# Kernel optimization log

Hardware: AMD Instinct MI355X
Metric: run time of the kernel (lower is better)

The kernel has to match this reference:

```python
import jax, jax.numpy as jnp
import numpy as np

T = 0.1        # temperature
MARGIN = 0.0   # margin m
NEG_IOU = 0.5  # negative iou threshold
K = 2          # pos_topk
WEIGHT = 1.0


def _l2norm(x, eps=1e-12):
    n = jnp.sqrt(jnp.sum(x * x, axis=-1, keepdims=True))
    return x / jnp.maximum(n, eps)


def setup_inputs() -> dict:
    key = jax.random.key(0)
    k0, k1, k2, k3 = jax.random.split(key, 4)
    B, C, N = 8, 256, 128
    s_per, m_per = 4, 2          # sentences per video, targets per sentence
    S, M = B * s_per, B * s_per * m_per
    video_feats = jax.random.normal(k0, (B, C, N, N), dtype=jnp.float32)
    sents_feats = jax.random.normal(k1, (S, C), dtype=jnp.float32)
    num_sentences = jnp.full((B,), s_per, dtype=jnp.int32)
    num_targets = jnp.full((S,), m_per, dtype=jnp.int32)
    iou2d = jax.random.uniform(k2, (S, N, N), dtype=jnp.float32)
    iou2ds = jax.random.uniform(k3, (M, N, N), dtype=jnp.float32)
    mask2d = jnp.asarray(np.triu(np.ones((N, N), dtype=bool)))
    return {"video_feats": video_feats, "sents_feats": sents_feats,
            "num_sentences": num_sentences, "num_targets": num_targets,
            "iou2d": iou2d, "iou2ds": iou2ds, "mask2d": mask2d}


def reference(video_feats, sents_feats, num_sentences, num_targets, iou2d, iou2ds, mask2d):
    B, C, N, _ = video_feats.shape
    S = iou2d.shape[0]
    M = iou2ds.shape[0]
    P = N * (N + 1) // 2  # number of valid proposals in upper-triangular mask2d
    flat_idx = jnp.nonzero(mask2d.reshape(-1), size=P)[0]

    # masked_select -> (B, P, C) proposal features, l2-normalized over C
    vf = video_feats.reshape(B, C, N * N)[:, :, flat_idx].transpose(0, 2, 1)
    vf = _l2norm(vf)
    sf = _l2norm(sents_feats)  # normalized as in original (unused downstream)
    iou2d_p = iou2d.reshape(S, -1)[:, flat_idx]    # (S, P)
    iou2ds_p = iou2ds.reshape(M, -1)[:, flat_idx]  # (M, P)

    s_per = S // B  # uniform sentences per video (static)
    m_per = M // S  # uniform targets per sentence (static)
    scatter_s2v = jnp.repeat(jnp.arange(B), s_per)    # (S,)
    scatter_m2s = jnp.repeat(jnp.arange(S), m_per)    # (M,)
    scatter_m2v = scatter_s2v[scatter_m2s]            # (M,)

    # top-K proposals per target moment by iou2ds
    topk_idx = jax.lax.top_k(iou2ds_p, K)[1]  # (M, K)
    topk_feats = jnp.take_along_axis(vf[scatter_m2v], topk_idx[:, :, None], axis=1)  # (M,K,C)
    pos_feats = topk_feats.reshape(M * K, C)

    # all (ref, pos) pairs within each sentence's m_per*K selected proposals
    mK = m_per * K
    a = jnp.arange(mK)
    shifts = jnp.arange(S) * mK
    ref_idx = (shifts[:, None] + jnp.repeat(a, mK)[None, :]).reshape(-1)  # (E,)
    pos_idx = (shifts[:, None] + jnp.tile(a, mK)[None, :]).reshape(-1)    # (E,)
    scatter_e2s = jnp.repeat(jnp.arange(S), mK * mK)                      # (E,)

    intra_pos = jnp.sum(pos_feats[ref_idx] * pos_feats[pos_idx], axis=-1)  # (E,)
    intra_all = pos_feats @ vf.reshape(-1, C).T                            # (M*K, B*P)

    # neg mask: within own video, exclude proposals with iou > NEG_IOU; other videos all negative
    own = scatter_s2v[:, None] == jnp.arange(B)[None, :]                   # (S, B)
    pos_mask = (own[:, :, None] & (iou2d_p > NEG_IOU)[:, None, :]).reshape(S, B * P)
    neg_mask = ~pos_mask

    ps = intra_pos
    all_s = intra_all[ref_idx]           # (E, B*P)
    nm = neg_mask[scatter_e2s]           # (E, B*P)
    pos_exp = jnp.exp((ps - MARGIN) / T)
    neg_sum = jnp.sum(jnp.exp(all_s / T) * nm, axis=-1)
    loss = jnp.mean(-((ps - MARGIN) / T - jnp.log(pos_exp + neg_sum)))
    return loss * WEIGHT
```

## Files before the change

kernel.cpp:

```cpp
#include <hip/hip_runtime.h>
#include <math.h>

#define NN    128
#define NN2   16384
#define CDIM  256
#define BV    8
#define MM    64
#define RR    128
#define PP    8256
#define NBLK  1032
#define BPB   129
#define TEMP  0.1f
#define NEGIOU 0.5f

typedef __attribute__((ext_vector_type(8))) short bf16x8;
typedef __attribute__((ext_vector_type(4))) float f32x4;

static __device__ __forceinline__ unsigned short f2bf(float x) {
    union { float f; unsigned u; } c; c.f = x;
    unsigned r = c.u + 0x7FFFu + ((c.u >> 16) & 1u);
    return (unsigned short)(r >> 16);
}

__global__ __launch_bounds__(256) void topk_part_kernel(const float* __restrict__ iou2ds,
                                                        float* __restrict__ pv,
                                                        int* __restrict__ pk) {
    int m = blockIdx.x, q = blockIdx.y, tid = threadIdx.x;
    const float* src = iou2ds + (size_t)m * NN2;
    float v1 = -1e30f, v2 = -1e30f;
    int k1 = 0x7fffffff, k2 = 0x7fffffff;
    int base = q * 4096;
#pragma unroll
    for (int i = 0; i < 16; ++i) {
        int k = base + tid + 256 * i;
        int r = k >> 7, c = k & 127;
        if (c < r) continue;
        float v = src[k];
        if (v > v1 || (v == v1 && k < k1)) { v2 = v1; k2 = k1; v1 = v; k1 = k; }
        else if (v > v2 || (v == v2 && k < k2)) { v2 = v; k2 = k; }
    }
    __shared__ float sv[512];  __shared__ int sk[512];
    __shared__ float sv2[128]; __shared__ int sk2[128];
    sv[tid * 2] = v1; sv[tid * 2 + 1] = v2;
    sk[tid * 2] = k1; sk[tid * 2 + 1] = k2;
    __syncthreads();
    if (tid < 64) {
        float b1 = -1e30f, b2 = -1e30f; int c1 = 0x7fffffff, c2 = 0x7fffffff;
        for (int t = tid * 8; t < tid * 8 + 8; ++t) {
            float v = sv[t]; int k = sk[t];
            if (v > b1 || (v == b1 && k < c1)) { b2 = b1; c2 = c1; b1 = v; c1 = k; }
            else if (v > b2 || (v == b2 && k < c2)) { b2 = v; c2 = k; }
        }
        sv2[tid * 2] = b1; sv2[tid * 2 + 1] = b2;
        sk2[tid * 2] = c1; sk2[tid * 2 + 1] = c2;
    }
    __syncthreads();
    if (tid == 0) {
        float b1 = -1e30f, b2 = -1e30f; int c1 = 0x7fffffff, c2 = 0x7fffffff;
        for (int t = 0; t < 128; ++t) {
            float v = sv2[t]; int k = sk2[t];
            if (v > b1 || (v == b1 && k < c1)) { b2 = b1; c2 = c1; b1 = v; c1 = k; }
            else if (v > b2 || (v == b2 && k < c2)) { b2 = v; c2 = k; }
        }
        pv[(m * 4 + q) * 2] = b1; pv[(m * 4 + q) * 2 + 1] = b2;
        pk[(m * 4 + q) * 2] = c1; pk[(m * 4 + q) * 2 + 1] = c2;
    }
}

__global__ __launch_bounds__(64) void posfeat_kernel(const float* __restrict__ vfeat,
                                                     const float* __restrict__ pv,
                                                     const int* __restrict__ pk,
                                                     float* __restrict__ pos,
                                                     unsigned short* __restrict__ posFrag) {
    int r = blockIdx.x, lane = threadIdx.x;
    int m = r >> 1, b = m >> 3, kk = r & 1;
    float b1 = -1e30f, b2 = -1e30f; int c1 = 0x7fffffff, c2 = 0x7fffffff;
    for (int t = 0; t < 8; ++t) {
        float v = pv[m * 8 + t]; int k = pk[m * 8 + t];
        if (v > b1 || (v == b1 && k < c1)) { b2 = b1; c2 = c1; b1 = v; c1 = k; }
        else if (v > b2 || (v == b2 && k < c2)) { b2 = v; c2 = k; }
    }
    int ij = kk ? c2 : c1;
    const float* base = vfeat + (size_t)b * CDIM * NN2 + ij;
    float v[4];
    float ss = 0.0f;
#pragma unroll
    for (int q = 0; q < 4; ++q) {
        int c = lane + 64 * q;
        v[q] = base[(size_t)c * NN2];
        ss += v[q] * v[q];
    }
#pragma unroll
    for (int o = 32; o > 0; o >>= 1) ss += __shfl_xor(ss, o, 64);
    float inv = 1.0f / fmaxf(sqrtf(ss), 1e-12f);
#pragma unroll
    for (int q = 0; q < 4; ++q) {
        int c = lane + 64 * q;
        float val = v[q] * inv;
        pos[r * CDIM + c] = val;
        int idx = (((c >> 5) * 8 + (r >> 4)) * 64 + ((r & 15) | (((c >> 3) & 3) << 4))) * 8 + (c & 7);
        posFrag[idx] = f2bf(val);
    }
}

__global__ __launch_bounds__(512, 4) void neg_kernel(const float* __restrict__ vfeat,
                                                     const float* __restrict__ iou2d,
                                                     const unsigned short* __restrict__ posFrag,
                                                     float* __restrict__ part) {
    __shared__ unsigned short sB[2][2][4][64][8];
    __shared__ int   sIJ[64];
    __shared__ int   sMask[64];
    __shared__ float sNP[8][64];
    __shared__ float sInv[64];
    __shared__ float sNeg[RR];

    int tid = threadIdx.x;
    int bid = blockIdx.x;
    int b   = bid / BPB;
    int p0  = (bid - b * BPB) * 64;

    if (tid < RR) sNeg[tid] = 0.0f;
    if (tid < 64) {
        int p = p0 + tid;
        int i = (int)((257.0f - sqrtf(66049.0f - 8.0f * (float)p)) * 0.5f);
        if (i < 0) i = 0;
        while ((i + 1) * (257 - (i + 1)) / 2 <= p) ++i;
        while (i * (257 - i) / 2 > p) --i;
        int j = p - i * (257 - i) / 2 + i;
        int ij = i * NN + j;
        sIJ[tid] = ij;
        int mask = 0;
#pragma unroll
        for (int t = 0; t < 4; ++t) {
            float iv = iou2d[((size_t)(4 * b + t)) * NN2 + ij];
            mask |= (iv > NEGIOU) ? (1 << t) : 0;
        }
        sMask[tid] = mask;
    }

    int lane = tid & 63;
    int col  = tid & 63;
    int wv   = tid >> 6;
    int rowgroup = wv >> 1;
    int colgroup = wv & 1;

    bf16x8 afrag[2][8];
    const bf16x8* pf = (const bf16x8*)posFrag;
#pragma unroll
    for (int mt = 0; mt < 2; ++mt)
#pragma unroll
        for (int s = 0; s < 8; ++s)
            afrag[mt][s] = pf[(s * 8 + rowgroup * 2 + mt) * 64 + lane];

    __syncthreads();

    const float* vcol = vfeat + (size_t)b * CDIM * NN2 + sIJ[col];

    f32x4 acc[2][2];
#pragma unroll
    for (int mt = 0; mt < 2; ++mt)
#pragma unroll
        for (int nt = 0; nt < 2; ++nt)
#pragma unroll
            for (int e = 0; e < 4; ++e) acc[mt][nt][e] = 0.0f;

    float nrm = 0.0f;
    float r[8];
#pragma unroll
    for (int j = 0; j < 8; ++j) r[j] = vcol[(size_t)(wv * 8 + j) * NN2];

    int s_loc = wv >> 2;
    int slot  = (col & 15) | ((wv & 3) << 4);
    int nt_w  = col >> 4;

    for (int ph = 0; ph < 4; ++ph) {
        union { bf16x8 v; unsigned u[4]; } pkd;
#pragma unroll
        for (int j = 0; j < 4; ++j)
            pkd.u[j] = (unsigned)f2bf(r[2 * j]) | ((unsigned)f2bf(r[2 * j + 1]) << 16);
#pragma unroll
        for (int j = 0; j < 8; ++j) nrm = fmaf(r[j], r[j], nrm);
        *(bf16x8*)&sB[ph & 1][s_loc][nt_w][slot][0] = pkd.v;
        __syncthreads();
        if (ph < 3) {
#pragma unroll
            for (int j = 0; j < 8; ++j)
                r[j] = vcol[(size_t)((ph + 1) * 64 + wv * 8 + j) * NN2];
        }
#pragma unroll
        for (int s = 0; s < 2; ++s)
#pragma unroll
            for (int ntl = 0; ntl < 2; ++ntl) {
                bf16x8 bfrag = *(const bf16x8*)&sB[ph & 1][s][colgroup * 2 + ntl][lane][0];
#pragma unroll
                for (int mt = 0; mt < 2; ++mt)
                    acc[mt][ntl] = __builtin_amdgcn_mfma_f32_16x16x32_bf16(
                        afrag[mt][ph * 2 + s], bfrag, acc[mt][ntl], 0, 0, 0);
            }
    }

    sNP[wv][col] = nrm;
    __syncthreads();
    if (tid < 64) {
        float s = 0.0f;
        for (int t = 0; t < 8; ++t) s += sNP[t][tid];
        sInv[tid] = 10.0f / fmaxf(sqrtf(s), 1e-12f);
    }
    __syncthreads();

#pragma unroll
    for (int mt = 0; mt < 2; ++mt)
#pragma unroll
        for (int ntl = 0; ntl < 2; ++ntl)
#pragma unroll
            for (int reg = 0; reg < 4; ++reg) {
                int row = rowgroup * 32 + mt * 16 + ((lane >> 4) << 2) + reg;
                int cl  = colgroup * 32 + ntl * 16 + (lane & 15);
                float e = __expf(acc[mt][ntl][reg] * sInv[cl]);
                int excl = ((row >> 4) == b) & ((sMask[cl] >> ((row >> 2) & 3)) & 1);
                e = excl ? 0.0f : e;
#pragma unroll
                for (int off = 1; off < 16; off <<= 1) e += __shfl_xor(e, off, 64);
                if ((lane & 15) == 0) atomicAdd(&sNeg[row], e);
            }
    __syncthreads();
    if (tid < RR) part[(size_t)tid * NBLK + bid] = sNeg[tid];
}

__global__ __launch_bounds__(256) void reduce_kernel(const float* __restrict__ part,
                                                     float* __restrict__ neg) {
    int r = blockIdx.x, tid = threadIdx.x;
    const float* row = part + (size_t)r * NBLK;
    float s = 0.0f;
    for (int t = tid; t < NBLK; t += 256) s += row[t];
#pragma unroll
    for (int o = 32; o > 0; o >>= 1) s += __shfl_xor(s, o, 64);
    __shared__ float sw[4];
    if ((tid & 63) == 0) sw[tid >> 6] = s;
    __syncthreads();
    if (tid == 0) neg[r] = sw[0] + sw[1] + sw[2] + sw[3];
}

__global__ __launch_bounds__(256) void loss_kernel(const float* __restrict__ pos,
                                                   const float* __restrict__ neg,
                                                   float* __restrict__ out) {
    int tid = threadIdx.x;
    float local = 0.0f;
    for (int e = tid; e < 512; e += 256) {
        int s  = e >> 4;
        int aa = (e >> 2) & 3;
        int bb = e & 3;
        int rr = s * 4 + aa;
        int pp = s * 4 + bb;
        const float4* pr = (const float4*)(pos + rr * CDIM);
        const float4* pq = (const float4*)(pos + pp * CDIM);
        float dot = 0.0f;
        for (int c = 0; c < CDIM / 4; ++c) {
            float4 a = pr[c], bv = pq[c];
            dot += a.x * bv.x + a.y * bv.y + a.z * bv.z + a.w * bv.w;
        }
        float x = dot / TEMP;
        local += logf(__expf(x) + neg[rr]) - x;
    }
#pragma unroll
    for (int o = 32; o > 0; o >>= 1) local += __shfl_xor(local, o, 64);
    __shared__ float sred[4];
    if ((tid & 63) == 0) sred[tid >> 6] = local;
    __syncthreads();
    if (tid == 0) out[0] = (sred[0] + sred[1] + sred[2] + sred[3]) / 512.0f;
}

extern "C" void kernel_launch(void* const* d_in, const int* in_sizes, int n_in,
                              void* d_out, int out_size, void* d_ws, size_t ws_size,
                              hipStream_t stream) {
    (void)in_sizes; (void)n_in; (void)out_size; (void)ws_size;
    const float* vfeat  = (const float*)d_in[0];
    const float* iou2d  = (const float*)d_in[4];
    const float* iou2ds = (const float*)d_in[5];

    float* ws = (float*)d_ws;
    float*          pos     = ws;
    unsigned short* posFrag = (unsigned short*)(ws + 32768);
    float*          pv      = ws + 32768 + 16384;
    int*            pk      = (int*)(pv + 512);
    float*          part    = pv + 1024;
    float*          neg     = part + RR * NBLK;

    topk_part_kernel<<<dim3(MM, 4), 256, 0, stream>>>(iou2ds, pv, pk);
    posfeat_kernel  <<<RR, 64, 0, stream>>>(vfeat, pv, pk, pos, posFrag);
    neg_kernel      <<<NBLK, 512, 0, stream>>>(vfeat, iou2d, posFrag, part);
    reduce_kernel   <<<RR, 256, 0, stream>>>(part, neg);
    loss_kernel     <<<1, 256, 0, stream>>>(pos, neg, (float*)d_out);
}
```

Baseline: 257.0 us.

## Fuse topk with posfeat and reduce with loss via last-block atomic counter

```diff
diff --git a/kernel.cpp b/kernel.cpp
--- a/kernel.cpp
+++ b/kernel.cpp
@@ -22,25 +22,27 @@
     return (unsigned short)(r >> 16);
 }
 
-__global__ __launch_bounds__(256) void topk_part_kernel(const float* __restrict__ iou2ds,
-                                                        float* __restrict__ pv,
-                                                        int* __restrict__ pk) {
-    int m = blockIdx.x, q = blockIdx.y, tid = threadIdx.x;
+__global__ __launch_bounds__(256) void prep_kernel(const float* __restrict__ vfeat,
+                                                   const float* __restrict__ iou2ds,
+                                                   float* __restrict__ pos,
+                                                   unsigned short* __restrict__ posFrag,
+                                                   int* __restrict__ done) {
+    int m = blockIdx.x, tid = threadIdx.x;
+    if (m == 0 && tid == 0) *done = 0;
+
     const float* src = iou2ds + (size_t)m * NN2;
     float v1 = -1e30f, v2 = -1e30f;
     int k1 = 0x7fffffff, k2 = 0x7fffffff;
-    int base = q * 4096;
-#pragma unroll
-    for (int i = 0; i < 16; ++i) {
-        int k = base + tid + 256 * i;
-        int r = k >> 7, c = k & 127;
-        if (c < r) continue;
+    for (int k = tid; k < NN2; k += 256) {
+        int i = k >> 7, j = k & 127;
+        if (j < i) continue;
         float v = src[k];
         if (v > v1 || (v == v1 && k < k1)) { v2 = v1; k2 = k1; v1 = v; k1 = k; }
         else if (v > v2 || (v == v2 && k < k2)) { v2 = v; k2 = k; }
     }
     __shared__ float sv[512];  __shared__ int sk[512];
     __shared__ float sv2[128]; __shared__ int sk2[128];
+    __shared__ int sTop[2];
     sv[tid * 2] = v1; sv[tid * 2 + 1] = v2;
     sk[tid * 2] = k1; sk[tid * 2 + 1] = k2;
     __syncthreads();
@@ -62,45 +64,33 @@
             if (v > b1 || (v == b1 && k < c1)) { b2 = b1; c2 = c1; b1 = v; c1 = k; }
             else if (v > b2 || (v == b2 && k < c2)) { b2 = v; c2 = k; }
         }
-        pv[(m * 4 + q) * 2] = b1; pv[(m * 4 + q) * 2 + 1] = b2;
-        pk[(m * 4 + q) * 2] = c1; pk[(m * 4 + q) * 2 + 1] = c2;
-    }
-}
-
-__global__ __launch_bounds__(64) void posfeat_kernel(const float* __restrict__ vfeat,
-                                                     const float* __restrict__ pv,
-                                                     const int* __restrict__ pk,
-                                                     float* __restrict__ pos,
-                                                     unsigned short* __restrict__ posFrag) {
-    int r = blockIdx.x, lane = threadIdx.x;
-    int m = r >> 1, b = m >> 3, kk = r & 1;
-    float b1 = -1e30f, b2 = -1e30f; int c1 = 0x7fffffff, c2 = 0x7fffffff;
-    for (int t = 0; t < 8; ++t) {
-        float v = pv[m * 8 + t]; int k = pk[m * 8 + t];
-        if (v > b1 || (v == b1 && k < c1)) { b2 = b1; c2 = c1; b1 = v; c1 = k; }
-        else if (v > b2 || (v == b2 && k < c2)) { b2 = v; c2 = k; }
-    }
-    int ij = kk ? c2 : c1;
+        sTop[0] = c1; sTop[1] = c2;
+    }
+    __syncthreads();
+
+    int rloc = tid >> 7;
+    int cloc = tid & 127;
+    int r = m * 2 + rloc;
+    int b = m >> 3;
+    int ij = sTop[rloc];
     const float* base = vfeat + (size_t)b * CDIM * NN2 + ij;
-    float v[4];
-    float ss = 0.0f;
-#pragma unroll
-    for (int q = 0; q < 4; ++q) {
-        int c = lane + 64 * q;
-        v[q] = base[(size_t)c * NN2];
-        ss += v[q] * v[q];
-    }
+    float va = base[(size_t)cloc * NN2];
+    float vb = base[(size_t)(cloc + 128) * NN2];
+    float ss = va * va + vb * vb;
 #pragma unroll
     for (int o = 32; o > 0; o >>= 1) ss += __shfl_xor(ss, o, 64);
-    float inv = 1.0f / fmaxf(sqrtf(ss), 1e-12f);
-#pragma unroll
-    for (int q = 0; q < 4; ++q) {
-        int c = lane + 64 * q;
-        float val = v[q] * inv;
-        pos[r * CDIM + c] = val;
-        int idx = (((c >> 5) * 8 + (r >> 4)) * 64 + ((r & 15) | (((c >> 3) & 3) << 4))) * 8 + (c & 7);
-        posFrag[idx] = f2bf(val);
-    }
+    __shared__ float sW[4];
+    if ((tid & 63) == 0) sW[tid >> 6] = ss;
+    __syncthreads();
+    float inv = 1.0f / fmaxf(sqrtf(sW[rloc * 2] + sW[rloc * 2 + 1]), 1e-12f);
+    float x0 = va * inv, x1 = vb * inv;
+    pos[r * CDIM + cloc] = x0;
+    pos[r * CDIM + cloc + 128] = x1;
+    int c0 = cloc, c1c = cloc + 128;
+    int i0 = (((c0 >> 5) * 8 + (r >> 4)) * 64 + ((r & 15) | (((c0 >> 3) & 3) << 4))) * 8 + (c0 & 7);
+    int i1 = (((c1c >> 5) * 8 + (r >> 4)) * 64 + ((r & 15) | (((c1c >> 3) & 3) << 4))) * 8 + (c1c & 7);
+    posFrag[i0] = f2bf(x0);
+    posFrag[i1] = f2bf(x1);
 }
 
 __global__ __launch_bounds__(512, 4) void neg_kernel(const float* __restrict__ vfeat,
@@ -227,8 +217,11 @@
     if (tid < RR) part[(size_t)tid * NBLK + bid] = sNeg[tid];
 }
 
-__global__ __launch_bounds__(256) void reduce_kernel(const float* __restrict__ part,
-                                                     float* __restrict__ neg) {
+__global__ __launch_bounds__(256) void finish_kernel(const float* __restrict__ part,
+                                                     const float* __restrict__ pos,
+                                                     float* __restrict__ neg,
+                                                     int* __restrict__ done,
+                                                     float* __restrict__ out) {
     int r = blockIdx.x, tid = threadIdx.x;
     const float* row = part + (size_t)r * NBLK;
     float s = 0.0f;
@@ -236,22 +229,25 @@
 #pragma unroll
     for (int o = 32; o > 0; o >>= 1) s += __shfl_xor(s, o, 64);
     __shared__ float sw[4];
+    __shared__ int amLast;
     if ((tid & 63) == 0) sw[tid >> 6] = s;
     __syncthreads();
-    if (tid == 0) neg[r] = sw[0] + sw[1] + sw[2] + sw[3];
-}
-
-__global__ __launch_bounds__(256) void loss_kernel(const float* __restrict__ pos,
-                                                   const float* __restrict__ neg,
-                                                   float* __restrict__ out) {
-    int tid = threadIdx.x;
+    if (tid == 0) {
+        float v = sw[0] + sw[1] + sw[2] + sw[3];
+        __hip_atomic_store(&neg[r], v, __ATOMIC_RELEASE, __HIP_MEMORY_SCOPE_AGENT);
+        int prev = __hip_atomic_fetch_add(done, 1, __ATOMIC_ACQ_REL, __HIP_MEMORY_SCOPE_AGENT);
+        amLast = (prev == RR - 1);
+    }
+    __syncthreads();
+    if (!amLast) return;
+
     float local = 0.0f;
     for (int e = tid; e < 512; e += 256) {
-        int s  = e >> 4;
+        int si = e >> 4;
         int aa = (e >> 2) & 3;
         int bb = e & 3;
-        int rr = s * 4 + aa;
-        int pp = s * 4 + bb;
+        int rr = si * 4 + aa;
+        int pp = si * 4 + bb;
         const float4* pr = (const float4*)(pos + rr * CDIM);
         const float4* pq = (const float4*)(pos + pp * CDIM);
         float dot = 0.0f;
@@ -260,7 +256,8 @@
             dot += a.x * bv.x + a.y * bv.y + a.z * bv.z + a.w * bv.w;
         }
         float x = dot / TEMP;
-        local += logf(__expf(x) + neg[rr]) - x;
+        float ns = __hip_atomic_load(&neg[rr], __ATOMIC_ACQUIRE, __HIP_MEMORY_SCOPE_AGENT);
+        local += logf(__expf(x) + ns) - x;
     }
 #pragma unroll
     for (int o = 32; o > 0; o >>= 1) local += __shfl_xor(local, o, 64);
@@ -281,14 +278,11 @@
     float* ws = (float*)d_ws;
     float*          pos     = ws;
     unsigned short* posFrag = (unsigned short*)(ws + 32768);
-    float*          pv      = ws + 32768 + 16384;
-    int*            pk      = (int*)(pv + 512);
-    float*          part    = pv + 1024;
+    float*          part    = ws + 32768 + 16384;
     float*          neg     = part + RR * NBLK;
-
-    topk_part_kernel<<<dim3(MM, 4), 256, 0, stream>>>(iou2ds, pv, pk);
-    posfeat_kernel  <<<RR, 64, 0, stream>>>(vfeat, pv, pk, pos, posFrag);
-    neg_kernel      <<<NBLK, 512, 0, stream>>>(vfeat, iou2d, posFrag, part);
-    reduce_kernel   <<<RR, 256, 0, stream>>>(part, neg);
-    loss_kernel     <<<1, 256, 0, stream>>>(pos, neg, (float*)d_out);
-}
+    int*            done    = (int*)(neg + RR);
+
+    prep_kernel  <<<MM, 256, 0, stream>>>(vfeat, iou2ds, pos, posFrag, done);
+    neg_kernel   <<<NBLK, 512, 0, stream>>>(vfeat, iou2d, posFrag, part);
+    finish_kernel<<<RR, 256, 0, stream>>>(part, pos, neg, done, (float*)d_out);
+}
```

New measurement: 285.6 us. 1.11x slower.
